# Kernel tuning notes

Measured on AMD Instinct MI355X. Metric: run time of the kernel, lower is better.

Reference implementation:

```python
import jax, jax.numpy as jnp
import numpy as np

N_NODES = 25000
N_EDGES = 800000
NUM_GRAPHS = 512
EMB = 128
OUT_EMB = 256
NUM_RADIAL = 6
NUM_DENSE = 3
NUM_TARGETS = 12


def setup_inputs() -> dict:
    key = jax.random.key(0)
    ks = jax.random.split(key, 10)
    m = jax.random.normal(ks[0], (N_EDGES, EMB), dtype=jnp.float32)
    rbf = jax.random.normal(ks[1], (N_EDGES, NUM_RADIAL), dtype=jnp.float32)
    edge_src = jax.random.randint(ks[2], (N_EDGES,), 0, N_NODES, dtype=jnp.int32)
    node2graph = jnp.sort(jax.random.randint(ks[3], (N_NODES,), 0, NUM_GRAPHS, dtype=jnp.int32))
    w_rbf = jax.random.normal(ks[4], (NUM_RADIAL, EMB), dtype=jnp.float32) * 0.4
    w_up = jax.random.normal(ks[5], (EMB, OUT_EMB), dtype=jnp.float32) * 0.08
    w_dense = jax.random.normal(ks[6], (NUM_DENSE, OUT_EMB, OUT_EMB), dtype=jnp.float32) * 0.06
    b_dense = jax.random.normal(ks[7], (NUM_DENSE, OUT_EMB), dtype=jnp.float32) * 0.01
    w_final = jax.random.normal(ks[8], (OUT_EMB, NUM_TARGETS), dtype=jnp.float32) * 0.05
    return {"m": m, "rbf": rbf, "edge_src": edge_src, "node2graph": node2graph,
            "w_rbf": w_rbf, "w_up": w_up, "w_dense": w_dense, "b_dense": b_dense,
            "w_final": w_final, "num_graphs": NUM_GRAPHS}


def reference(m, rbf, edge_src, node2graph, w_rbf, w_up, w_dense, b_dense, w_final, num_graphs):
    n_nodes = node2graph.shape[0]
    # edge: tmp = m * dense_rbf(rbf)   [E, emb]
    tmp = m * (rbf @ w_rbf)
    # reverse graph + copy_e/sum == scatter-sum per-edge tmp into original src node
    t = jax.ops.segment_sum(tmp, edge_src, num_segments=n_nodes)  # [N, emb]
    # up projection (no bias)
    t = t @ w_up  # [N, out_emb]
    # dense layers with swish activation
    for i in range(w_dense.shape[0]):
        t = jax.nn.silu(t @ w_dense[i] + b_dense[i])
    # final projection (no bias)
    t = t @ w_final  # [N, num_targets]
    # extensive readout: per-graph sum over nodes
    return jax.ops.segment_sum(t, node2graph, num_segments=num_graphs)  # [G, num_targets]
```

## Files before the change

kernel.cpp:

```cpp
#include <hip/hip_runtime.h>
#include <hip/hip_bf16.h>
#include <math.h>

#define EMB 128
#define OUT 256
#define RAD 6
#define NDL 3
#define NTGT 12
#define MT 32
#define S 264

typedef __attribute__((ext_vector_type(8))) short short8;
typedef __attribute__((ext_vector_type(4))) float floatx4;

__device__ inline short f2bf(float x) {
    __hip_bfloat16 h = __float2bfloat16(x);
    return *reinterpret_cast<short*>(&h);
}


__global__ void hist_kernel(const int* __restrict__ src, int* __restrict__ counts, int E) {
    int i = blockIdx.x * blockDim.x + threadIdx.x;
    if (i < E) atomicAdd(&counts[src[i]], 1);
}

__global__ void scan_kernel(const int* __restrict__ counts, int* __restrict__ offs,
                            int* __restrict__ cursor, int N) {
    __shared__ int sums[1024];
    int tid = threadIdx.x;
    int chunk = (N + 1023) / 1024;
    int beg = tid * chunk;
    int end = min(beg + chunk, N);
    int s = 0;
    for (int i = beg; i < end; i++) s += counts[i];
    int mysum = s;
    sums[tid] = s;
    __syncthreads();
    for (int off = 1; off < 1024; off <<= 1) {
        int add = (tid >= off) ? sums[tid - off] : 0;
        __syncthreads();
        sums[tid] += add;
        __syncthreads();
    }
    int prefix = sums[tid] - mysum;
    for (int i = beg; i < end; i++) {
        int c = counts[i];
        offs[i] = prefix;
        cursor[i] = prefix;
        prefix += c;
    }
    if (tid == 0) offs[N] = sums[1023];
}

__global__ void scatter_kernel(const int* __restrict__ src, int* __restrict__ cursor,
                               int* __restrict__ eids, int E) {
    int i = blockIdx.x * blockDim.x + threadIdx.x;
    if (i < E) {
        int pos = atomicAdd(&cursor[src[i]], 1);
        eids[pos] = i;
    }
}


__global__ void prep_kernel(const float* __restrict__ w_up, const float* __restrict__ w_dense,
                            const float* __restrict__ w_final,
                            short* __restrict__ w_upT, short* __restrict__ w_dT,
                            short* __restrict__ w_fT) {
    const int T1 = OUT * EMB;
    const int T2 = NDL * OUT * OUT;
    const int T3 = 16 * OUT;
    int total = T1 + T2 + T3;
    for (int i = blockIdx.x * blockDim.x + threadIdx.x; i < total; i += gridDim.x * blockDim.x) {
        if (i < T1) {
            int n = i >> 7, k = i & 127;
            w_upT[i] = f2bf(w_up[k * OUT + n]);
        } else if (i < T1 + T2) {
            int j = i - T1;
            int l = j >> 16, o = (j >> 8) & 255, k = j & 255;
            w_dT[j] = f2bf(w_dense[(l << 16) + (k << 8) + o]);
        } else {
            int j = i - T1 - T2;
            int t = j >> 8, k = j & 255;
            w_fT[j] = (t < NTGT) ? f2bf(w_final[k * NTGT + t]) : (short)0;
        }
    }
}


__global__ void gather_kernel(const float* __restrict__ m, const float* __restrict__ rbf,
                              const float* __restrict__ w_rbf,
                              const int* __restrict__ offs, const int* __restrict__ eids,
                              __hip_bfloat16* __restrict__ t0, int N) {
    int n = blockIdx.x;
    int tid = threadIdx.x;
    float wr[RAD];
#pragma unroll
    for (int r = 0; r < RAD; r++) wr[r] = w_rbf[r * EMB + tid];

    int b = offs[n], e = offs[n + 1];
    float acc = 0.f;
    int idx = b;
    for (; idx + 4 <= e; idx += 4) {
        int e0 = eids[idx], e1 = eids[idx + 1], e2 = eids[idx + 2], e3 = eids[idx + 3];
        float c0 = 0.f, c1 = 0.f, c2 = 0.f, c3 = 0.f;
#pragma unroll
        for (int r = 0; r < RAD; r++) {
            c0 += rbf[(size_t)e0 * RAD + r] * wr[r];
            c1 += rbf[(size_t)e1 * RAD + r] * wr[r];
            c2 += rbf[(size_t)e2 * RAD + r] * wr[r];
            c3 += rbf[(size_t)e3 * RAD + r] * wr[r];
        }
        float m0 = m[(size_t)e0 * EMB + tid];
        float m1 = m[(size_t)e1 * EMB + tid];
        float m2 = m[(size_t)e2 * EMB + tid];
        float m3 = m[(size_t)e3 * EMB + tid];
        acc += m0 * c0 + m1 * c1 + m2 * c2 + m3 * c3;
    }
    for (; idx < e; idx++) {
        int e0 = eids[idx];
        float c0 = 0.f;
#pragma unroll
        for (int r = 0; r < RAD; r++) c0 += rbf[(size_t)e0 * RAD + r] * wr[r];
        acc += m[(size_t)e0 * EMB + tid] * c0;
    }
    t0[(size_t)n * EMB + tid] = __float2bfloat16(acc);
}


__global__ __launch_bounds__(256) void chain_kernel(
    const __hip_bfloat16* __restrict__ t0,
    const short* __restrict__ w_upT, const short* __restrict__ w_dT,
    const float* __restrict__ b_dense, const short* __restrict__ w_fT,
    const int* __restrict__ node2graph, float* __restrict__ out, int N) {

    __shared__ short sA[2][MT * S];

    int tid = threadIdx.x;
    int n0 = blockIdx.x * MT;
    int wave = tid >> 6, lane = tid & 63;
    int lo = lane & 15;
    int quad = lane >> 4;
    int kq = quad * 8;
    int wcol = wave * 64;

    {
        int r = tid >> 3;
        int c = (tid & 7) * 16;
        uint4 v0 = {0, 0, 0, 0}, v1 = {0, 0, 0, 0};
        if (n0 + r < N) {
            const uint4* src = (const uint4*)((const short*)t0 + (size_t)(n0 + r) * EMB + c);
            v0 = src[0];
            v1 = src[1];
        }
        *(uint4*)&sA[0][r * S + c] = v0;
        *(uint4*)&sA[0][r * S + c + 8] = v1;
    }
    __syncthreads();

    auto layer = [&](int cur, int K, const short* __restrict__ Bt,
                     const float* __restrict__ bias, bool act) {
        floatx4 acc[2][4];
#pragma unroll
        for (int mt = 0; mt < 2; mt++)
#pragma unroll
            for (int nt = 0; nt < 4; nt++)
                acc[mt][nt] = floatx4{0.f, 0.f, 0.f, 0.f};

        for (int kc = 0; kc < K; kc += 32) {
            short8 a0 = *(const short8*)&sA[cur][(lo) * S + kc + kq];
            short8 a1 = *(const short8*)&sA[cur][(16 + lo) * S + kc + kq];
#pragma unroll
            for (int nt = 0; nt < 4; nt++) {
                int n = wcol + nt * 16 + lo;
                short8 b = *(const short8*)&Bt[(size_t)n * K + kc + kq];
                acc[0][nt] = __builtin_amdgcn_mfma_f32_16x16x32_bf16(a0, b, acc[0][nt], 0, 0, 0);
                acc[1][nt] = __builtin_amdgcn_mfma_f32_16x16x32_bf16(a1, b, acc[1][nt], 0, 0, 0);
            }
        }

        float bv[4];
#pragma unroll
        for (int nt = 0; nt < 4; nt++) bv[nt] = bias ? bias[wcol + nt * 16 + lo] : 0.f;

        short* dst = sA[cur ^ 1];
#pragma unroll
        for (int mt = 0; mt < 2; mt++)
#pragma unroll
            for (int nt = 0; nt < 4; nt++) {
                int n = wcol + nt * 16 + lo;
#pragma unroll
                for (int i = 0; i < 4; i++) {
                    int mrow = mt * 16 + quad * 4 + i;
                    float x = acc[mt][nt][i] + bv[nt];
                    if (act) x = x / (1.f + __expf(-x));
                    dst[mrow * S + n] = f2bf(x);
                }
            }
        __syncthreads();
    };

    layer(0, EMB, w_upT, nullptr, false);
    layer(1, OUT, w_dT + 0 * OUT * OUT, b_dense + 0 * OUT, true);
    layer(0, OUT, w_dT + 1 * OUT * OUT, b_dense + 1 * OUT, true);
    layer(1, OUT, w_dT + 2 * OUT * OUT, b_dense + 2 * OUT, true);

    if (wave == 0) {
        floatx4 facc[2];
        facc[0] = floatx4{0.f, 0.f, 0.f, 0.f};
        facc[1] = floatx4{0.f, 0.f, 0.f, 0.f};
        for (int kc = 0; kc < OUT; kc += 32) {
            short8 a0 = *(const short8*)&sA[0][(lo) * S + kc + kq];
            short8 a1 = *(const short8*)&sA[0][(16 + lo) * S + kc + kq];
            short8 b = *(const short8*)&w_fT[lo * OUT + kc + kq];
            facc[0] = __builtin_amdgcn_mfma_f32_16x16x32_bf16(a0, b, facc[0], 0, 0, 0);
            facc[1] = __builtin_amdgcn_mfma_f32_16x16x32_bf16(a1, b, facc[1], 0, 0, 0);
        }
        if (lo < NTGT) {
#pragma unroll
            for (int mt = 0; mt < 2; mt++)
#pragma unroll
                for (int i = 0; i < 4; i++) {
                    int node = n0 + mt * 16 + quad * 4 + i;
                    if (node < N)
                        atomicAdd(&out[node2graph[node] * NTGT + lo], facc[mt][i]);
                }
        }
    }
}


extern "C" void kernel_launch(void* const* d_in, const int* in_sizes, int n_in,
                              void* d_out, int out_size, void* d_ws, size_t ws_size,
                              hipStream_t stream) {
    const float* m        = (const float*)d_in[0];
    const float* rbf      = (const float*)d_in[1];
    const int*   edge_src = (const int*)d_in[2];
    const int*   node2g   = (const int*)d_in[3];
    const float* w_rbf    = (const float*)d_in[4];
    const float* w_up     = (const float*)d_in[5];
    const float* w_dense  = (const float*)d_in[6];
    const float* b_dense  = (const float*)d_in[7];
    const float* w_final  = (const float*)d_in[8];

    int E = in_sizes[2];
    int N = in_sizes[3];
    float* out = (float*)d_out;

    char* p = (char*)d_ws;
    auto alloc = [&](size_t bytes) {
        char* r = p;
        p += (bytes + 255) & ~(size_t)255;
        return r;
    };
    int*   counts = (int*)alloc((size_t)N * 4);
    int*   offs   = (int*)alloc((size_t)(N + 1) * 4);
    int*   cursor = (int*)alloc((size_t)N * 4);
    int*   eids   = (int*)alloc((size_t)E * 4);
    __hip_bfloat16* t0 = (__hip_bfloat16*)alloc((size_t)N * EMB * 2);
    short* w_upT  = (short*)alloc((size_t)OUT * EMB * 2);
    short* w_dT   = (short*)alloc((size_t)NDL * OUT * OUT * 2);
    short* w_fT   = (short*)alloc((size_t)16 * OUT * 2);

    hipMemsetAsync(counts, 0, (size_t)N * 4, stream);
    hipMemsetAsync(d_out, 0, (size_t)out_size * 4, stream);

    prep_kernel<<<512, 256, 0, stream>>>(w_up, w_dense, w_final, w_upT, w_dT, w_fT);
    hist_kernel<<<(E + 255) / 256, 256, 0, stream>>>(edge_src, counts, E);
    scan_kernel<<<1, 1024, 0, stream>>>(counts, offs, cursor, N);
    scatter_kernel<<<(E + 255) / 256, 256, 0, stream>>>(edge_src, cursor, eids, E);
    gather_kernel<<<N, EMB, 0, stream>>>(m, rbf, w_rbf, offs, eids, t0, N);
    chain_kernel<<<(N + MT - 1) / MT, 256, 0, stream>>>(t0, w_upT, w_dT, b_dense,
                                                        w_fT, node2g, out, N);
}
```

Before: 773.8 us.

## Restructure edge gather into four edge groups with float4 loads and reduction

The per-node gather now splits its 128 threads into four 32-lane groups, each handling a different edge with float4 loads of m and vectorized rbf loads. Edge ids are staged in shared memory per chunk, and the per-group partial sums are combined with a cross-half shuffle plus a shared-memory reduction. The aim is more memory-level parallelism, with more edges in flight and wider loads, in this bandwidth-bound gather. In exchange it adds extra barriers and a reduction step per node, and each lane recomputes four rbf dot products per edge.

New measurement: 764.3 us. About the same (-1.2%).

```diff
diff --git a/kernel.cpp b/kernel.cpp
--- a/kernel.cpp
+++ b/kernel.cpp
@@ -9,6 +9,7 @@
 #define NTGT 12
 #define MT 32
 #define S 264
+#define ECH 1024
 
 typedef __attribute__((ext_vector_type(8))) short short8;
 typedef __attribute__((ext_vector_type(4))) float floatx4;
@@ -87,43 +88,91 @@
 }
 
 
-__global__ void gather_kernel(const float* __restrict__ m, const float* __restrict__ rbf,
-                              const float* __restrict__ w_rbf,
-                              const int* __restrict__ offs, const int* __restrict__ eids,
-                              __hip_bfloat16* __restrict__ t0, int N) {
+__global__ __launch_bounds__(128) void gather_kernel(
+    const float* __restrict__ m, const float* __restrict__ rbf,
+    const float* __restrict__ w_rbf,
+    const int* __restrict__ offs, const int* __restrict__ eids,
+    __hip_bfloat16* __restrict__ t0, int N) {
+
+    __shared__ int sEid[ECH];
+    __shared__ float sRed[32 * 4];
+
     int n = blockIdx.x;
     int tid = threadIdx.x;
-    float wr[RAD];
-#pragma unroll
-    for (int r = 0; r < RAD; r++) wr[r] = w_rbf[r * EMB + tid];
+    int grp = tid >> 5;
+    int c = tid & 31;
+
+    float4 wq[RAD];
+#pragma unroll
+    for (int r = 0; r < RAD; r++) wq[r] = *(const float4*)&w_rbf[r * EMB + 4 * c];
 
     int b = offs[n], e = offs[n + 1];
-    float acc = 0.f;
-    int idx = b;
-    for (; idx + 4 <= e; idx += 4) {
-        int e0 = eids[idx], e1 = eids[idx + 1], e2 = eids[idx + 2], e3 = eids[idx + 3];
-        float c0 = 0.f, c1 = 0.f, c2 = 0.f, c3 = 0.f;
-#pragma unroll
-        for (int r = 0; r < RAD; r++) {
-            c0 += rbf[(size_t)e0 * RAD + r] * wr[r];
-            c1 += rbf[(size_t)e1 * RAD + r] * wr[r];
-            c2 += rbf[(size_t)e2 * RAD + r] * wr[r];
-            c3 += rbf[(size_t)e3 * RAD + r] * wr[r];
-        }
-        float m0 = m[(size_t)e0 * EMB + tid];
-        float m1 = m[(size_t)e1 * EMB + tid];
-        float m2 = m[(size_t)e2 * EMB + tid];
-        float m3 = m[(size_t)e3 * EMB + tid];
-        acc += m0 * c0 + m1 * c1 + m2 * c2 + m3 * c3;
-    }
-    for (; idx < e; idx++) {
-        int e0 = eids[idx];
-        float c0 = 0.f;
-#pragma unroll
-        for (int r = 0; r < RAD; r++) c0 += rbf[(size_t)e0 * RAD + r] * wr[r];
-        acc += m[(size_t)e0 * EMB + tid] * c0;
-    }
-    t0[(size_t)n * EMB + tid] = __float2bfloat16(acc);
+    float ax = 0.f, ay = 0.f, az = 0.f, aw = 0.f;
+
+    for (int base = b; base < e; base += ECH) {
+        int cnt = min(ECH, e - base);
+        __syncthreads();
+        for (int i = tid; i < cnt; i += 128) sEid[i] = eids[base + i];
+        __syncthreads();
+
+        int i = grp;
+        for (; i + 8 <= cnt; i += 8) {
+            int e0 = sEid[i], e1 = sEid[i + 4];
+            const float* rb0 = &rbf[(size_t)e0 * RAD];
+            const float* rb1 = &rbf[(size_t)e1 * RAD];
+            float2 p0 = *(const float2*)&rb0[0];
+            float2 p1 = *(const float2*)&rb0[2];
+            float2 p2 = *(const float2*)&rb0[4];
+            float2 q0 = *(const float2*)&rb1[0];
+            float2 q1 = *(const float2*)&rb1[2];
+            float2 q2 = *(const float2*)&rb1[4];
+            float4 m0 = *(const float4*)&m[(size_t)e0 * EMB + 4 * c];
+            float4 m1 = *(const float4*)&m[(size_t)e1 * EMB + 4 * c];
+
+            float cx0 = wq[0].x * p0.x + wq[1].x * p0.y + wq[2].x * p1.x + wq[3].x * p1.y + wq[4].x * p2.x + wq[5].x * p2.y;
+            float cy0 = wq[0].y * p0.x + wq[1].y * p0.y + wq[2].y * p1.x + wq[3].y * p1.y + wq[4].y * p2.x + wq[5].y * p2.y;
+            float cz0 = wq[0].z * p0.x + wq[1].z * p0.y + wq[2].z * p1.x + wq[3].z * p1.y + wq[4].z * p2.x + wq[5].z * p2.y;
+            float cw0 = wq[0].w * p0.x + wq[1].w * p0.y + wq[2].w * p1.x + wq[3].w * p1.y + wq[4].w * p2.x + wq[5].w * p2.y;
+            ax += m0.x * cx0; ay += m0.y * cy0; az += m0.z * cz0; aw += m0.w * cw0;
+
+            float cx1 = wq[0].x * q0.x + wq[1].x * q0.y + wq[2].x * q1.x + wq[3].x * q1.y + wq[4].x * q2.x + wq[5].x * q2.y;
+            float cy1 = wq[0].y * q0.x + wq[1].y * q0.y + wq[2].y * q1.x + wq[3].y * q1.y + wq[4].y * q2.x + wq[5].y * q2.y;
+            float cz1 = wq[0].z * q0.x + wq[1].z * q0.y + wq[2].z * q1.x + wq[3].z * q1.y + wq[4].z * q2.x + wq[5].z * q2.y;
+            float cw1 = wq[0].w * q0.x + wq[1].w * q0.y + wq[2].w * q1.x + wq[3].w * q1.y + wq[4].w * q2.x + wq[5].w * q2.y;
+            ax += m1.x * cx1; ay += m1.y * cy1; az += m1.z * cz1; aw += m1.w * cw1;
+        }
+        for (; i < cnt; i += 4) {
+            int e0 = sEid[i];
+            const float* rb0 = &rbf[(size_t)e0 * RAD];
+            float2 p0 = *(const float2*)&rb0[0];
+            float2 p1 = *(const float2*)&rb0[2];
+            float2 p2 = *(const float2*)&rb0[4];
+            float4 m0 = *(const float4*)&m[(size_t)e0 * EMB + 4 * c];
+            float cx0 = wq[0].x * p0.x + wq[1].x * p0.y + wq[2].x * p1.x + wq[3].x * p1.y + wq[4].x * p2.x + wq[5].x * p2.y;
+            float cy0 = wq[0].y * p0.x + wq[1].y * p0.y + wq[2].y * p1.x + wq[3].y * p1.y + wq[4].y * p2.x + wq[5].y * p2.y;
+            float cz0 = wq[0].z * p0.x + wq[1].z * p0.y + wq[2].z * p1.x + wq[3].z * p1.y + wq[4].z * p2.x + wq[5].z * p2.y;
+            float cw0 = wq[0].w * p0.x + wq[1].w * p0.y + wq[2].w * p1.x + wq[3].w * p1.y + wq[4].w * p2.x + wq[5].w * p2.y;
+            ax += m0.x * cx0; ay += m0.y * cy0; az += m0.z * cz0; aw += m0.w * cw0;
+        }
+    }
+
+    ax += __shfl_xor(ax, 32); ay += __shfl_xor(ay, 32);
+    az += __shfl_xor(az, 32); aw += __shfl_xor(aw, 32);
+    __syncthreads();
+    if (tid >= 64 && tid < 96) {
+        sRed[c * 4 + 0] = ax; sRed[c * 4 + 1] = ay;
+        sRed[c * 4 + 2] = az; sRed[c * 4 + 3] = aw;
+    }
+    __syncthreads();
+    if (tid < 32) {
+        ax += sRed[c * 4 + 0]; ay += sRed[c * 4 + 1];
+        az += sRed[c * 4 + 2]; aw += sRed[c * 4 + 3];
+        __hip_bfloat16* dst = t0 + (size_t)n * EMB + 4 * c;
+        dst[0] = __float2bfloat16(ax);
+        dst[1] = __float2bfloat16(ay);
+        dst[2] = __float2bfloat16(az);
+        dst[3] = __float2bfloat16(aw);
+    }
 }
 
 
@@ -268,7 +317,7 @@
     hist_kernel<<<(E + 255) / 256, 256, 0, stream>>>(edge_src, counts, E);
     scan_kernel<<<1, 1024, 0, stream>>>(counts, offs, cursor, N);
     scatter_kernel<<<(E + 255) / 256, 256, 0, stream>>>(edge_src, cursor, eids, E);
-    gather_kernel<<<N, EMB, 0, stream>>>(m, rbf, w_rbf, offs, eids, t0, N);
+    gather_kernel<<<N, 128, 0, stream>>>(m, rbf, w_rbf, offs, eids, t0, N);
     chain_kernel<<<(N + MT - 1) / MT, 256, 0, stream>>>(t0, w_upT, w_dT, b_dense,
                                                         w_fT, node2g, out, N);
 }
```

## Balance gather across waves with edge-range chunks and atomic segment flushes

Applied to the files above, without the earlier changes.

The gather step moves from one block per node to a fixed grid in which each wave processes an equal contiguous range of the sorted edge list. Each half-wave accumulates float4 columns for runs of edges that share a node and flushes them with atomicAdd into a zeroed fp32 node buffer. A pos2node array is written during scatter to support this, and loads for upcoming edges are software-prefetched. The aim is to remove load imbalance from uneven node degrees and the per-node launch overhead. The cost is extra atomics at chunk and node boundaries, a memset of the fp32 buffer, doubled intermediate traffic, and a bf16 conversion moved into chain_kernel.

Result: slower. 810.2 us (+4.7%).

```diff
diff --git a/kernel.cpp b/kernel.cpp
--- a/kernel.cpp
+++ b/kernel.cpp
@@ -9,6 +9,7 @@
 #define NTGT 12
 #define MT 32
 #define S 264
+#define GBLK 1536
 
 typedef __attribute__((ext_vector_type(8))) short short8;
 typedef __attribute__((ext_vector_type(4))) float floatx4;
@@ -53,11 +54,13 @@
 }
 
 __global__ void scatter_kernel(const int* __restrict__ src, int* __restrict__ cursor,
-                               int* __restrict__ eids, int E) {
+                               int* __restrict__ eids, int* __restrict__ pos2node, int E) {
     int i = blockIdx.x * blockDim.x + threadIdx.x;
     if (i < E) {
-        int pos = atomicAdd(&cursor[src[i]], 1);
+        int s = src[i];
+        int pos = atomicAdd(&cursor[s], 1);
         eids[pos] = i;
+        pos2node[pos] = s;
     }
 }
 
@@ -87,48 +90,82 @@
 }
 
 
-__global__ void gather_kernel(const float* __restrict__ m, const float* __restrict__ rbf,
-                              const float* __restrict__ w_rbf,
-                              const int* __restrict__ offs, const int* __restrict__ eids,
-                              __hip_bfloat16* __restrict__ t0, int N) {
-    int n = blockIdx.x;
+__global__ __launch_bounds__(256, 6) void gather_kernel(
+    const float* __restrict__ m, const float* __restrict__ rbf,
+    const float* __restrict__ w_rbf,
+    const int* __restrict__ eids, const int* __restrict__ pos2node,
+    float* __restrict__ t0, int E) {
+
     int tid = threadIdx.x;
-    float wr[RAD];
-#pragma unroll
-    for (int r = 0; r < RAD; r++) wr[r] = w_rbf[r * EMB + tid];
-
-    int b = offs[n], e = offs[n + 1];
-    float acc = 0.f;
-    int idx = b;
-    for (; idx + 4 <= e; idx += 4) {
-        int e0 = eids[idx], e1 = eids[idx + 1], e2 = eids[idx + 2], e3 = eids[idx + 3];
-        float c0 = 0.f, c1 = 0.f, c2 = 0.f, c3 = 0.f;
-#pragma unroll
-        for (int r = 0; r < RAD; r++) {
-            c0 += rbf[(size_t)e0 * RAD + r] * wr[r];
-            c1 += rbf[(size_t)e1 * RAD + r] * wr[r];
-            c2 += rbf[(size_t)e2 * RAD + r] * wr[r];
-            c3 += rbf[(size_t)e3 * RAD + r] * wr[r];
-        }
-        float m0 = m[(size_t)e0 * EMB + tid];
-        float m1 = m[(size_t)e1 * EMB + tid];
-        float m2 = m[(size_t)e2 * EMB + tid];
-        float m3 = m[(size_t)e3 * EMB + tid];
-        acc += m0 * c0 + m1 * c1 + m2 * c2 + m3 * c3;
-    }
-    for (; idx < e; idx++) {
-        int e0 = eids[idx];
-        float c0 = 0.f;
-#pragma unroll
-        for (int r = 0; r < RAD; r++) c0 += rbf[(size_t)e0 * RAD + r] * wr[r];
-        acc += m[(size_t)e0 * EMB + tid] * c0;
-    }
-    t0[(size_t)n * EMB + tid] = __float2bfloat16(acc);
+    int lane = tid & 63;
+    int grp = lane >> 5;
+    int c = lane & 31;
+    int gwave = blockIdx.x * 4 + (tid >> 6);
+    int nW = gridDim.x * 4;
+    int chunk = (E + nW - 1) / nW;
+    int p0 = gwave * chunk;
+    int p1 = min(p0 + chunk, E);
+
+    float4 wq[RAD];
+#pragma unroll
+    for (int r = 0; r < RAD; r++) wq[r] = *(const float4*)&w_rbf[r * EMB + 4 * c];
+
+    float ax = 0.f, ay = 0.f, az = 0.f, aw = 0.f;
+    int prev = -1;
+
+    int p = p0 + grp;
+    if (p < p1) {
+        int eidA = eids[p];
+        int nodeA = pos2node[p];
+        int pB = min(p + 2, E - 1);
+        int eidB = eids[pB];
+        int nodeB = pos2node[pB];
+        float4 mv = *(const float4*)&m[(size_t)eidA * EMB + 4 * c];
+        const float* rr = &rbf[(size_t)eidA * RAD];
+        float2 r0 = *(const float2*)&rr[0];
+        float2 r1 = *(const float2*)&rr[2];
+        float2 r2 = *(const float2*)&rr[4];
+
+        for (; p < p1; p += 2) {
+            int pC = min(p + 4, E - 1);
+            int eidC = eids[pC];
+            int nodeC = pos2node[pC];
+            float4 mvB = *(const float4*)&m[(size_t)eidB * EMB + 4 * c];
+            const float* rrB = &rbf[(size_t)eidB * RAD];
+            float2 s0 = *(const float2*)&rrB[0];
+            float2 s1 = *(const float2*)&rrB[2];
+            float2 s2 = *(const float2*)&rrB[4];
+
+            if (nodeA != prev) {
+                if (prev >= 0) {
+                    float* dst = &t0[(size_t)prev * EMB + 4 * c];
+                    atomicAdd(&dst[0], ax); atomicAdd(&dst[1], ay);
+                    atomicAdd(&dst[2], az); atomicAdd(&dst[3], aw);
+                }
+                ax = ay = az = aw = 0.f;
+                prev = nodeA;
+            }
+
+            float cx = wq[0].x*r0.x + wq[1].x*r0.y + wq[2].x*r1.x + wq[3].x*r1.y + wq[4].x*r2.x + wq[5].x*r2.y;
+            float cy = wq[0].y*r0.x + wq[1].y*r0.y + wq[2].y*r1.x + wq[3].y*r1.y + wq[4].y*r2.x + wq[5].y*r2.y;
+            float cz = wq[0].z*r0.x + wq[1].z*r0.y + wq[2].z*r1.x + wq[3].z*r1.y + wq[4].z*r2.x + wq[5].z*r2.y;
+            float cw = wq[0].w*r0.x + wq[1].w*r0.y + wq[2].w*r1.x + wq[3].w*r1.y + wq[4].w*r2.x + wq[5].w*r2.y;
+            ax += mv.x * cx; ay += mv.y * cy; az += mv.z * cz; aw += mv.w * cw;
+
+            mv = mvB; r0 = s0; r1 = s1; r2 = s2;
+            nodeA = nodeB; nodeB = nodeC; eidB = eidC;
+        }
+        if (prev >= 0) {
+            float* dst = &t0[(size_t)prev * EMB + 4 * c];
+            atomicAdd(&dst[0], ax); atomicAdd(&dst[1], ay);
+            atomicAdd(&dst[2], az); atomicAdd(&dst[3], aw);
+        }
+    }
 }
 
 
 __global__ __launch_bounds__(256) void chain_kernel(
-    const __hip_bfloat16* __restrict__ t0,
+    const float* __restrict__ t0,
     const short* __restrict__ w_upT, const short* __restrict__ w_dT,
     const float* __restrict__ b_dense, const short* __restrict__ w_fT,
     const int* __restrict__ node2graph, float* __restrict__ out, int N) {
@@ -145,15 +182,22 @@
 
     {
         int r = tid >> 3;
-        int c = (tid & 7) * 16;
-        uint4 v0 = {0, 0, 0, 0}, v1 = {0, 0, 0, 0};
+        int ccol = (tid & 7) * 16;
+        short vals[16];
         if (n0 + r < N) {
-            const uint4* src = (const uint4*)((const short*)t0 + (size_t)(n0 + r) * EMB + c);
-            v0 = src[0];
-            v1 = src[1];
-        }
-        *(uint4*)&sA[0][r * S + c] = v0;
-        *(uint4*)&sA[0][r * S + c + 8] = v1;
+            const float* src = &t0[(size_t)(n0 + r) * EMB + ccol];
+#pragma unroll
+            for (int j = 0; j < 16; j += 4) {
+                float4 f = *(const float4*)&src[j];
+                vals[j + 0] = f2bf(f.x); vals[j + 1] = f2bf(f.y);
+                vals[j + 2] = f2bf(f.z); vals[j + 3] = f2bf(f.w);
+            }
+        } else {
+#pragma unroll
+            for (int j = 0; j < 16; j++) vals[j] = 0;
+        }
+        *(uint4*)&sA[0][r * S + ccol] = *(uint4*)&vals[0];
+        *(uint4*)&sA[0][r * S + ccol + 8] = *(uint4*)&vals[8];
     }
     __syncthreads();
 
@@ -252,23 +296,25 @@
         p += (bytes + 255) & ~(size_t)255;
         return r;
     };
-    int*   counts = (int*)alloc((size_t)N * 4);
-    int*   offs   = (int*)alloc((size_t)(N + 1) * 4);
-    int*   cursor = (int*)alloc((size_t)N * 4);
-    int*   eids   = (int*)alloc((size_t)E * 4);
-    __hip_bfloat16* t0 = (__hip_bfloat16*)alloc((size_t)N * EMB * 2);
-    short* w_upT  = (short*)alloc((size_t)OUT * EMB * 2);
-    short* w_dT   = (short*)alloc((size_t)NDL * OUT * OUT * 2);
-    short* w_fT   = (short*)alloc((size_t)16 * OUT * 2);
+    int*   counts   = (int*)alloc((size_t)N * 4);
+    int*   offs     = (int*)alloc((size_t)(N + 1) * 4);
+    int*   cursor   = (int*)alloc((size_t)N * 4);
+    int*   eids     = (int*)alloc((size_t)E * 4);
+    int*   pos2node = (int*)alloc((size_t)E * 4);
+    float* t0       = (float*)alloc((size_t)N * EMB * 4);
+    short* w_upT    = (short*)alloc((size_t)OUT * EMB * 2);
+    short* w_dT     = (short*)alloc((size_t)NDL * OUT * OUT * 2);
+    short* w_fT     = (short*)alloc((size_t)16 * OUT * 2);
 
     hipMemsetAsync(counts, 0, (size_t)N * 4, stream);
+    hipMemsetAsync(t0, 0, (size_t)N * EMB * 4, stream);
     hipMemsetAsync(d_out, 0, (size_t)out_size * 4, stream);
 
     prep_kernel<<<512, 256, 0, stream>>>(w_up, w_dense, w_final, w_upT, w_dT, w_fT);
     hist_kernel<<<(E + 255) / 256, 256, 0, stream>>>(edge_src, counts, E);
     scan_kernel<<<1, 1024, 0, stream>>>(counts, offs, cursor, N);
-    scatter_kernel<<<(E + 255) / 256, 256, 0, stream>>>(edge_src, cursor, eids, E);
-    gather_kernel<<<N, EMB, 0, stream>>>(m, rbf, w_rbf, offs, eids, t0, N);
+    scatter_kernel<<<(E + 255) / 256, 256, 0, stream>>>(edge_src, cursor, eids, pos2node, E);
+    gather_kernel<<<GBLK, 256, 0, stream>>>(m, rbf, w_rbf, eids, pos2node, t0, E);
     chain_kernel<<<(N + MT - 1) / MT, 256, 0, stream>>>(t0, w_upT, w_dT, b_dense,
                                                         w_fT, node2g, out, N);
 }
```
